# Kernel tuning notes

Measured on AMD Instinct MI355X. Metric: run time of the kernel, lower is better.

## Reference

```python
import jax, jax.numpy as jnp
import numpy as np

B, N, C, E, H, V, T = 64, 196, 512, 512, 1024, 10000, 20
NULL_IDX, START_IDX = 0, 1


def setup_inputs() -> dict:
    key = jax.random.key(0)
    ks = jax.random.split(key, 16)
    p = lambda k, s: jax.random.normal(k, s, jnp.float32) * 0.02
    z = lambda n: jnp.zeros((n,), jnp.float32)
    return dict(
        X=jax.random.normal(ks[0], (B, N, C), jnp.float32),
        emb=p(ks[1], (V, E)),
        W_ih=p(ks[2], (E + C, 4 * H)), b_ih=z(4 * H),
        W_hh=p(ks[3], (H, 4 * H)), b_hh=z(4 * H),
        Wa=p(ks[4], (C, H)), ba=z(H),          # attention lin_annotations
        Wh=p(ks[5], (H, H)), bh=z(H),          # attention lin_hidden
        Wo=p(ks[6], (H, 1)), bo=z(1),          # attention out
        Wlh=p(ks[7], (H, E)), blh=z(E),        # linear_hidden
        Wlc=p(ks[8], (C, E)), blc=z(E),        # linear_context
        Wout=p(ks[9], (E, V)), bout=z(V),      # linear_out
        Wc0=p(ks[10], (C, H)), bc0=z(H),       # cell_init
        Wh0=p(ks[11], (C, H)), bh0=z(H),       # hidden_init
    )


def reference(X, emb, W_ih, b_ih, W_hh, b_hh, Wa, ba, Wh, bh, Wo, bo,
              Wlh, blh, Wlc, blc, Wout, bout, Wc0, bc0, Wh0, bh0):
    Xm = jnp.mean(X, axis=1)                       # [B, C]
    c0 = jnp.tanh(Xm @ Wc0 + bc0)                  # [B, H]
    h0 = jnp.tanh(Xm @ Wh0 + bh0)                  # [B, H]
    Xa = X @ Wa + ba                               # [B, N, H] step-invariant annotation proj
    tok0 = jnp.full((B,), START_IDX, jnp.int32)

    def step(carry, _):
        tok, h, c = carry
        e = emb[tok]                                           # [B, E]
        att = jnp.tanh(Xa + (h @ Wh + bh)[:, None, :])          # [B, N, H]
        # softmax over a size-1 last axis -> weights == 1 (faithful to original)
        w = jax.nn.softmax(att @ Wo + bo, axis=-1)              # [B, N, 1]
        ctx = jnp.sum(w * X, axis=1)                            # [B, C]
        gates = jnp.concatenate([e, ctx], axis=1) @ W_ih + b_ih + h @ W_hh + b_hh
        gi, gf, gg, go = jnp.split(gates, 4, axis=1)            # torch LSTMCell gate order
        c2 = jax.nn.sigmoid(gf) * c + jax.nn.sigmoid(gi) * jnp.tanh(gg)
        h2 = jax.nn.sigmoid(go) * jnp.tanh(c2)
        comb = e + (h2 @ Wlh + blh) + (ctx @ Wlc + blc)         # [B, E]
        lp = jax.nn.log_softmax(comb @ Wout + bout, axis=-1)    # [B, V]
        tok2 = jnp.argmax(lp, axis=-1).astype(jnp.int32)
        return (tok2, h2, c2), lp

    _, lps = jax.lax.scan(step, (tok0, h0, c0), None, length=T - 1)  # [T-1, B, V]
    out0 = jnp.broadcast_to(jax.nn.one_hot(START_IDX, V, dtype=jnp.float32), (B, V))[None]
    out = jnp.concatenate([out0, lps], axis=0)                  # [T, B, V]
    return jnp.transpose(out, (1, 0, 2))                        # [B, T, V]
```

## Files before the change

kernel.cpp:

```cpp
#include <hip/hip_runtime.h>
#include <math.h>

typedef unsigned short u16;
typedef unsigned long long u64;
typedef __attribute__((ext_vector_type(8))) short bf16x8;
typedef __attribute__((ext_vector_type(4))) float f32x4;
typedef __attribute__((ext_vector_type(8))) unsigned short ushort8;

constexpr int kB = 64;
constexpr int kN = 196;
constexpr int kC = 512;
constexpr int kE = 512;
constexpr int kH = 1024;
constexpr int kV = 10000;
constexpr int kT = 20;
constexpr int kG4 = 4 * kH;
constexpr int kKA = 1536;
constexpr int kLT = 625;

__device__ __forceinline__ float sigmoidf_(float x) { return 1.0f / (1.0f + expf(-x)); }

__device__ __forceinline__ u16 f2bf(float x) {
    unsigned u = __float_as_uint(x);
    u += 0x7FFF + ((u >> 16) & 1);
    return (u16)(u >> 16);
}
__device__ __forceinline__ float bf2f(u16 u) {
    return __uint_as_float((unsigned)u << 16);
}
__device__ __forceinline__ void splitbf(float x, u16& hi, u16& lo) {
    hi = f2bf(x);
    lo = f2bf(x - bf2f(hi));
}

__device__ __forceinline__ u64 packMI(float M, int I) {
    unsigned mb = __float_as_uint(M);
    mb = (mb & 0x80000000u) ? ~mb : (mb | 0x80000000u);
    return ((u64)mb << 32) | (u64)(0xFFFFFFFFu - (unsigned)I);
}


__global__ __launch_bounds__(256) void k_colsum(const float* __restrict__ X,
                                                float* __restrict__ XsP) {
    int gid = blockIdx.x * 256 + threadIdx.x;
    int c = gid & 511, b = (gid >> 9) & 63, ch = gid >> 15;
    const float* p = X + (size_t)b * kN * kC + (size_t)(ch * 49) * kC + c;
    float s = 0.f;
    for (int n = 0; n < 49; ++n) s += p[(size_t)n * kC];
    XsP[gid] = s;
}

__global__ __launch_bounds__(256) void k_colred(const float* __restrict__ XsP,
                                                float* __restrict__ XsT) {
    int gid = blockIdx.x * 256 + threadIdx.x;
    int b = gid >> 9, c = gid & 511;
    float s = 0.f;
#pragma unroll
    for (int ch = 0; ch < 4; ++ch) s += XsP[ch * 32768 + b * 512 + c];
    XsT[c * kB + b] = s;
}

__global__ __launch_bounds__(256) void k_setupgemm(const float* __restrict__ XsT,
                                                   const float* __restrict__ W_ih,
                                                   const float* __restrict__ b_ih,
                                                   const float* __restrict__ b_hh,
                                                   const float* __restrict__ Wc0,
                                                   const float* __restrict__ bc0,
                                                   const float* __restrict__ Wh0,
                                                   const float* __restrict__ bh0,
                                                   const float* __restrict__ Wlc,
                                                   const float* __restrict__ blc,
                                                   const float* __restrict__ blh,
                                                   float* __restrict__ gbP,
                                                   float* __restrict__ cBJ,
                                                   u16* __restrict__ hb0Hi,
                                                   u16* __restrict__ hb0Lo,
                                                   float* __restrict__ ctxc) {
    __shared__ float4 wt4[64][8];
    int t = threadIdx.x;
    int b = t & 63, q = t >> 6;
    int tile = blockIdx.x;

    const float* W; const float* bias; float scale; int ldw; int mode; int j;
    if (tile < 128) {
        j = tile * 32; W = W_ih + (size_t)kE * kG4 + j; ldw = kG4;
        bias = nullptr; scale = 1.f; mode = 0;
    } else if (tile < 160) {
        j = (tile - 128) * 32; W = Wc0 + j; ldw = kH;
        bias = bc0 + j; scale = 1.0f / 196.0f; mode = 1;
    } else if (tile < 192) {
        j = (tile - 160) * 32; W = Wh0 + j; ldw = kH;
        bias = bh0 + j; scale = 1.0f / 196.0f; mode = 2;
    } else {
        j = (tile - 192) * 32; W = Wlc + j; ldw = kE;
        bias = blc + j; scale = 1.f; mode = 3;
    }

    int lr = t >> 2, lq2 = (t & 3) * 2;
    float acc[8];
#pragma unroll
    for (int i = 0; i < 8; ++i) acc[i] = 0.f;

    for (int kt = 0; kt < kC; kt += 64) {
        const float* wrow = W + (size_t)(kt + lr) * ldw;
        float4 w0 = *reinterpret_cast<const float4*>(wrow + lq2 * 4);
        float4 w1 = *reinterpret_cast<const float4*>(wrow + lq2 * 4 + 4);
        __syncthreads();
        wt4[lr][lq2] = w0; wt4[lr][lq2 + 1] = w1;
        __syncthreads();
        const float* ap = XsT + (size_t)kt * kB + b;
#pragma unroll 8
        for (int kk = 0; kk < 64; ++kk) {
            float a = ap[kk * 64] * scale;
            float4 u0 = wt4[kk][q * 2];
            float4 u1 = wt4[kk][q * 2 + 1];
            acc[0] += a * u0.x; acc[1] += a * u0.y; acc[2] += a * u0.z; acc[3] += a * u0.w;
            acc[4] += a * u1.x; acc[5] += a * u1.y; acc[6] += a * u1.z; acc[7] += a * u1.w;
        }
    }
#pragma unroll
    for (int cc = 0; cc < 8; ++cc) {
        int col = q * 8 + cc;
        float v = acc[cc];
        if (mode == 0) {
            int jsrc = j + col;
            v += b_ih[jsrc] + b_hh[jsrc];
            int nd = ((jsrc & 1023) << 2) | (jsrc >> 10);
            gbP[(size_t)b * kG4 + nd] = v;
        } else if (mode == 1) {
            v = tanhf(v + bias[col]);
            cBJ[(size_t)b * kH + j + col] = v;
        } else if (mode == 2) {
            v = tanhf(v + bias[col]);
            u16 hi, lo; splitbf(v, hi, lo);
            hb0Hi[(size_t)b * kH + j + col] = hi;
            hb0Lo[(size_t)b * kH + j + col] = lo;
        } else {
            v += bias[col] + blh[j + col];
            ctxc[(size_t)b * kE + j + col] = v;
        }
    }
}

__global__ __launch_bounds__(256) void k_wconv(const float* __restrict__ src,
                                               u16* __restrict__ dhi,
                                               u16* __restrict__ dlo,
                                               int ld, int n_valid, int pitch,
                                               int k_off, int nxTiles) {
    __shared__ float lds[64][65];
    int t = threadIdx.x;
    int nx = blockIdx.x % nxTiles, ky = blockIdx.x / nxTiles;
    int n0 = nx * 64, k0 = ky * 64;
    int c = t & 63, r0 = t >> 6;
#pragma unroll
    for (int i = 0; i < 16; ++i) {
        int r = r0 + i * 4;
        float v = (n0 + c < n_valid) ? src[(size_t)(k0 + r) * ld + n0 + c] : 0.f;
        lds[r][c] = v;
    }
    __syncthreads();
    int nl = t >> 2, kq = t & 3;
#pragma unroll
    for (int half = 0; half < 2; ++half) {
        ushort8 vh, vl;
#pragma unroll
        for (int jj = 0; jj < 8; ++jj) {
            u16 hi, lo; splitbf(lds[kq * 16 + half * 8 + jj][nl], hi, lo);
            vh[jj] = hi; vl[jj] = lo;
        }
        size_t o = (size_t)(n0 + nl) * pitch + k_off + k0 + kq * 16 + half * 8;
        *(ushort8*)(&dhi[o]) = vh;
        *(ushort8*)(&dlo[o]) = vl;
    }
}

__global__ __launch_bounds__(256) void k_wgconv(const float* __restrict__ src,
                                                u16* __restrict__ dhi,
                                                u16* __restrict__ dlo,
                                                int k_off) {
    __shared__ float lds[64][65];
    int t = threadIdx.x;
    int nx = blockIdx.x & 63, ky = blockIdx.x >> 6;
    int n0 = nx * 64, k0 = ky * 64;
    int c = t & 63, r0 = t >> 6;
#pragma unroll
    for (int i = 0; i < 16; ++i) {
        int r = r0 + i * 4;
        int nd = n0 + c;
        int nsrc = (nd & 3) * 1024 + (nd >> 2);
        lds[r][c] = src[(size_t)(k0 + r) * kG4 + nsrc];
    }
    __syncthreads();
    int nl = t >> 2, kq = t & 3;
#pragma unroll
    for (int half = 0; half < 2; ++half) {
        ushort8 vh, vl;
#pragma unroll
        for (int jj = 0; jj < 8; ++jj) {
            u16 hi, lo; splitbf(lds[kq * 16 + half * 8 + jj][nl], hi, lo);
            vh[jj] = hi; vl[jj] = lo;
        }
        size_t o = (size_t)(n0 + nl) * kKA + k_off + k0 + kq * 16 + half * 8;
        *(ushort8*)(&dhi[o]) = vh;
        *(ushort8*)(&dlo[o]) = vl;
    }
}

__global__ __launch_bounds__(256) void k_embconv(const float* __restrict__ emb,
                                                 u16* __restrict__ eh,
                                                 u16* __restrict__ el) {
    int gid = blockIdx.x * 256 + threadIdx.x;
    float4 v = *reinterpret_cast<const float4*>(emb + (size_t)gid * 4);
    u16 h0, l0, h1, l1, h2, l2, h3, l3;
    splitbf(v.x, h0, l0); splitbf(v.y, h1, l1);
    splitbf(v.z, h2, l2); splitbf(v.w, h3, l3);
    u64 ph = (u64)h0 | ((u64)h1 << 16) | ((u64)h2 << 32) | ((u64)h3 << 48);
    u64 pl = (u64)l0 | ((u64)l1 << 16) | ((u64)l2 << 32) | ((u64)l3 << 48);
    *reinterpret_cast<u64*>(eh + (size_t)gid * 4) = ph;
    *reinterpret_cast<u64*>(el + (size_t)gid * 4) = pl;
}

__global__ __launch_bounds__(256) void k_out0(float* __restrict__ out) {
    int gid = blockIdx.x * 256 + threadIdx.x;
    if (gid >= kB * kV) return;
    int b = gid / kV, v = gid - b * kV;
    out[(size_t)b * kT * kV + v] = (v == 1) ? 1.0f : 0.0f;
}


struct StepP {
    u16 *hbHi0, *hbLo0, *hbHi1, *hbLo1;
    float *cBJ, *gbP, *ctxc;
    u16 *CbHi, *CbLo;
    const u16 *WgHi, *WgLo, *WlhHi, *WlhLo, *WoHi, *WoLo, *embHi, *embLo;
    const float *bout;
    float *lbuf0, *lbuf1;
    float *Ssh;
    u64 *Mxsh;
    float *out;
};

__device__ __forceinline__ int resolveTok(const StepP& p, int step, int b) {
    if (step <= 1) return 1;
    int slot = (step - 1) & 1;
    u64 best = 0;
#pragma unroll
    for (int sh = 0; sh < 8; ++sh) {
        u64 v = p.Mxsh[(slot * 8 + sh) * 64 + b];
        if (v > best) best = v;
    }
    return (int)(0xFFFFFFFFu - (unsigned)(best & 0xFFFFFFFFu));
}

__global__ __launch_bounds__(256) void k_stepG(StepP p, int step) {
    __shared__ float sred[4][64][17];
    __shared__ int tok[64];
    const int blk = blockIdx.x, t = threadIdx.x;
    const int l = t & 63, w = t >> 6, la = l & 15, lg = l >> 4;
    const int Pb = (step - 1) & 1, Qb = step & 1;

    if (t < 64) tok[t] = resolveTok(p, step, t);
    if (blk < 8 && t < 64) {
        int slot = step & 1;
        p.Ssh[(slot * 8 + blk) * 64 + t] = 0.f;
        p.Mxsh[(slot * 8 + blk) * 64 + t] = 0;
    }
    __syncthreads();

    const u16* hpHi = Pb ? p.hbHi1 : p.hbHi0;
    const u16* hpLo = Pb ? p.hbLo1 : p.hbLo0;
    u16* nHi = Qb ? p.hbHi1 : p.hbHi0;
    u16* nLo = Qb ? p.hbLo1 : p.hbLo0;
    const int n0 = blk * 16;
    const int kb = w * 384 + lg * 8;
    const u16* wh = p.WgHi + (size_t)(n0 + la) * kKA + kb;
    const u16* wl = p.WgLo + (size_t)(n0 + la) * kKA + kb;
    int tk[4];
#pragma unroll
    for (int m = 0; m < 4; ++m) tk[m] = tok[m * 16 + la];

    f32x4 acc[4];
#pragma unroll
    for (int m = 0; m < 4; ++m) acc[m] = (f32x4){0.f, 0.f, 0.f, 0.f};
    for (int ks = 0; ks < 12; ++ks) {
        int kc = w * 384 + ks * 32;
        bf16x8 bhi = *(const bf16x8*)(wh + ks * 32);
        bf16x8 blo = *(const bf16x8*)(wl + ks * 32);
#pragma unroll
        for (int m = 0; m < 4; ++m) {
            int row = m * 16 + la;
            bf16x8 ahi8, alo8;
            if (kc < kE) {
                size_t o = (size_t)tk[m] * kE + kc + lg * 8;
                ahi8 = *(const bf16x8*)(p.embHi + o);
                alo8 = *(const bf16x8*)(p.embLo + o);
            } else {
                size_t o = (size_t)row * kH + (kc - kE) + lg * 8;
                ahi8 = *(const bf16x8*)(hpHi + o);
                alo8 = *(const bf16x8*)(hpLo + o);
            }
            acc[m] = __builtin_amdgcn_mfma_f32_16x16x32_bf16(ahi8, bhi, acc[m], 0, 0, 0);
            acc[m] = __builtin_amdgcn_mfma_f32_16x16x32_bf16(ahi8, blo, acc[m], 0, 0, 0);
            acc[m] = __builtin_amdgcn_mfma_f32_16x16x32_bf16(alo8, bhi, acc[m], 0, 0, 0);
        }
    }
#pragma unroll
    for (int m = 0; m < 4; ++m)
#pragma unroll
        for (int r = 0; r < 4; ++r)
            sred[w][m * 16 + lg * 4 + r][la] = acc[m][r];
    __syncthreads();
    int b = l, jl = w;
    float g[4];
#pragma unroll
    for (int gi = 0; gi < 4; ++gi) {
        int cc = jl * 4 + gi;
        g[gi] = sred[0][b][cc] + sred[1][b][cc] + sred[2][b][cc] + sred[3][b][cc]
              + p.gbP[(size_t)b * kG4 + n0 + cc];
    }
    int jp = blk * 4 + jl;
    float cold = p.cBJ[b * kH + jp];
    float c2 = sigmoidf_(g[1]) * cold + sigmoidf_(g[0]) * tanhf(g[2]);
    float h2 = sigmoidf_(g[3]) * tanhf(c2);
    p.cBJ[b * kH + jp] = c2;
    u16 hh, hl; splitbf(h2, hh, hl);
    nHi[(size_t)b * kH + jp] = hh;
    nLo[(size_t)b * kH + jp] = hl;
}

__global__ __launch_bounds__(256) void k_stepC(StepP p, int step) {
    __shared__ float sred[4][64][17];
    __shared__ int tok[64];
    __shared__ float lseArr[64];
    const int blk = blockIdx.x, t = threadIdx.x;
    const int Qb = step & 1;

    if (blk < 32) {
        if (t < 64) tok[t] = resolveTok(p, step, t);
        __syncthreads();
        const u16* hcHi = Qb ? p.hbHi1 : p.hbHi0;
        const u16* hcLo = Qb ? p.hbLo1 : p.hbLo0;
        const int l = t & 63, w = t >> 6, la = l & 15, lg = l >> 4;
        const int n0 = blk * 16;
        const int kb = w * 256 + lg * 8;
        const u16* wh = p.WlhHi + (size_t)(n0 + la) * kH + kb;
        const u16* wl = p.WlhLo + (size_t)(n0 + la) * kH + kb;
        f32x4 acc[4];
#pragma unroll
        for (int m = 0; m < 4; ++m) acc[m] = (f32x4){0.f, 0.f, 0.f, 0.f};
        for (int ks = 0; ks < 8; ++ks) {
            int ko = ks * 32;
            bf16x8 bhi = *(const bf16x8*)(wh + ko);
            bf16x8 blo = *(const bf16x8*)(wl + ko);
#pragma unroll
            for (int m = 0; m < 4; ++m) {
                size_t o = (size_t)(m * 16 + la) * kH + kb + ko;
                bf16x8 ahi8 = *(const bf16x8*)(hcHi + o);
                bf16x8 alo8 = *(const bf16x8*)(hcLo + o);
                acc[m] = __builtin_amdgcn_mfma_f32_16x16x32_bf16(ahi8, bhi, acc[m], 0, 0, 0);
                acc[m] = __builtin_amdgcn_mfma_f32_16x16x32_bf16(ahi8, blo, acc[m], 0, 0, 0);
                acc[m] = __builtin_amdgcn_mfma_f32_16x16x32_bf16(alo8, bhi, acc[m], 0, 0, 0);
            }
        }
#pragma unroll
        for (int m = 0; m < 4; ++m)
#pragma unroll
            for (int r = 0; r < 4; ++r)
                sred[w][m * 16 + lg * 4 + r][la] = acc[m][r];
        __syncthreads();
        int b = l, cq = w;
        int tokb = tok[b];
#pragma unroll
        for (int i = 0; i < 4; ++i) {
            int cc = cq * 4 + i;
            int col = (blk * 16) + cc;
            float v = sred[0][b][cc] + sred[1][b][cc] + sred[2][b][cc] + sred[3][b][cc];
            v += bf2f(p.embHi[(size_t)tokb * kE + col]) + bf2f(p.embLo[(size_t)tokb * kE + col]);
            v += p.ctxc[(size_t)b * kE + col];
            u16 hh, hl; splitbf(v, hh, hl);
            p.CbHi[(size_t)b * kE + col] = hh;
            p.CbLo[(size_t)b * kE + col] = hl;
        }
    } else if (step > 1) {
        int slot = (step - 1) & 1;
        if (t < 64) {
            float S = 0.f;
#pragma unroll
            for (int sh = 0; sh < 8; ++sh) S += p.Ssh[(slot * 8 + sh) * 64 + t];
            lseArr[t] = logf(S);
        }
        __syncthreads();
        const float* lb = slot ? p.lbuf1 : p.lbuf0;
        for (int idx = (blk - 32) * 256 + t; idx < kB * kV; idx += 224 * 256) {
            int b = idx / kV, c = idx - b * kV;
            __builtin_nontemporal_store(lb[(size_t)b * kV + c] - lseArr[b],
                                        &p.out[((size_t)b * kT + (step - 1)) * kV + c]);
        }
    }
}

__global__ __launch_bounds__(256) void k_stepL(StepP p, int step) {
    __shared__ float sred[4][64][17];
    __shared__ float redM[256], redS[256];
    __shared__ int redI[256];
    const int blk = blockIdx.x, t = threadIdx.x;
    const int l = t & 63, w = t >> 6, la = l & 15, lg = l >> 4;
    int slot = step & 1;
    float* lb = slot ? p.lbuf1 : p.lbuf0;
    int shard = blk & 7;
    const int c0 = blk * 16;
    const int kb = w * 128 + lg * 8;
    const u16* wh = p.WoHi + (size_t)(c0 + la) * kE + kb;
    const u16* wl = p.WoLo + (size_t)(c0 + la) * kE + kb;
    const u16* a0h = p.CbHi + (size_t)la * kE + kb;
    const u16* a0l = p.CbLo + (size_t)la * kE + kb;
    f32x4 acc[4];
#pragma unroll
    for (int m = 0; m < 4; ++m) acc[m] = (f32x4){0.f, 0.f, 0.f, 0.f};
#pragma unroll
    for (int ks = 0; ks < 4; ++ks) {
        int ko = ks * 32;
        bf16x8 bhi = *(const bf16x8*)(wh + ko);
        bf16x8 blo = *(const bf16x8*)(wl + ko);
#pragma unroll
        for (int m = 0; m < 4; ++m) {
            bf16x8 ahi8 = *(const bf16x8*)(a0h + (size_t)m * 16 * kE + ko);
            bf16x8 alo8 = *(const bf16x8*)(a0l + (size_t)m * 16 * kE + ko);
            acc[m] = __builtin_amdgcn_mfma_f32_16x16x32_bf16(ahi8, bhi, acc[m], 0, 0, 0);
            acc[m] = __builtin_amdgcn_mfma_f32_16x16x32_bf16(ahi8, blo, acc[m], 0, 0, 0);
            acc[m] = __builtin_amdgcn_mfma_f32_16x16x32_bf16(alo8, bhi, acc[m], 0, 0, 0);
        }
    }
#pragma unroll
    for (int m = 0; m < 4; ++m)
#pragma unroll
        for (int r = 0; r < 4; ++r)
            sred[w][m * 16 + lg * 4 + r][la] = acc[m][r];
    __syncthreads();
    int b = l, cq = w;
    float vals[4];
#pragma unroll
    for (int i = 0; i < 4; ++i) {
        int cc = cq * 4 + i;
        vals[i] = sred[0][b][cc] + sred[1][b][cc] + sred[2][b][cc] + sred[3][b][cc]
                + p.bout[c0 + cc];
    }
    __builtin_nontemporal_store((f32x4){vals[0], vals[1], vals[2], vals[3]},
                                (f32x4*)(lb + (size_t)b * kV + c0 + cq * 4));
    float m = vals[0]; int mi = 0;
#pragma unroll
    for (int i = 1; i < 4; ++i) if (vals[i] > m) { m = vals[i]; mi = i; }
    float se = 0.f;
#pragma unroll
    for (int i = 0; i < 4; ++i) se += __expf(vals[i] - m);
    redM[t] = m; redS[t] = se; redI[t] = c0 + cq * 4 + mi;
    __syncthreads();
    if (t < 64) {
        float M = redM[t], S = redS[t]; int I = redI[t];
#pragma unroll
        for (int q2 = 1; q2 < 4; ++q2) {
            float m2 = redM[t + q2 * 64], s2 = redS[t + q2 * 64];
            int i2 = redI[t + q2 * 64];
            float Mn = fmaxf(M, m2);
            S = S * __expf(M - Mn) + s2 * __expf(m2 - Mn);
            if (m2 > M || (m2 == M && i2 < I)) I = i2;
            M = Mn;
        }
        float S0 = S * __expf(M);
        atomicAdd(&p.Ssh[(slot * 8 + shard) * 64 + t], S0);
        atomicMax(&p.Mxsh[(slot * 8 + shard) * 64 + t], packMI(M, I));
    }
}

__global__ __launch_bounds__(256) void k_stepO(StepP p) {
    __shared__ float lseArr[64];
    const int blk = blockIdx.x, t = threadIdx.x;
    int slot = (kT - 1) & 1;
    if (t < 64) {
        float S = 0.f;
#pragma unroll
        for (int sh = 0; sh < 8; ++sh) S += p.Ssh[(slot * 8 + sh) * 64 + t];
        lseArr[t] = logf(S);
    }
    __syncthreads();
    const float* lb = slot ? p.lbuf1 : p.lbuf0;
    for (int idx = blk * 256 + t; idx < kB * kV; idx += 256 * 256) {
        int b = idx / kV, c = idx - b * kV;
        __builtin_nontemporal_store(lb[(size_t)b * kV + c] - lseArr[b],
                                    &p.out[((size_t)b * kT + (kT - 1)) * kV + c]);
    }
}


extern "C" void kernel_launch(void* const* d_in, const int* in_sizes, int n_in,
                              void* d_out, int out_size, void* d_ws, size_t ws_size,
                              hipStream_t stream) {
    const float* X    = (const float*)d_in[0];
    const float* emb  = (const float*)d_in[1];
    const float* W_ih = (const float*)d_in[2];
    const float* b_ih = (const float*)d_in[3];
    const float* W_hh = (const float*)d_in[4];
    const float* b_hh = (const float*)d_in[5];
    const float* Wlh  = (const float*)d_in[12];
    const float* blh  = (const float*)d_in[13];
    const float* Wlc  = (const float*)d_in[14];
    const float* blc  = (const float*)d_in[15];
    const float* Wout = (const float*)d_in[16];
    const float* bout = (const float*)d_in[17];
    const float* Wc0  = (const float*)d_in[18];
    const float* bc0  = (const float*)d_in[19];
    const float* Wh0  = (const float*)d_in[20];
    const float* bh0  = (const float*)d_in[21];
    float* out = (float*)d_out;

    char* cur = (char*)d_ws;
    auto carve = [&](size_t bytes) { char* p = cur; cur += (bytes + 255) & ~(size_t)255; return p; };

    u16* hbHi0 = (u16*)carve((size_t)kB * kH * 2);
    u16* hbLo0 = (u16*)carve((size_t)kB * kH * 2);
    u16* hbHi1 = (u16*)carve((size_t)kB * kH * 2);
    u16* hbLo1 = (u16*)carve((size_t)kB * kH * 2);
    float* cBJ  = (float*)carve((size_t)kB * kH * 4);
    float* gbP  = (float*)carve((size_t)kB * kG4 * 4);
    float* ctxc = (float*)carve((size_t)kB * kE * 4);
    u16* CbHi   = (u16*)carve((size_t)kB * kE * 2);
    u16* CbLo   = (u16*)carve((size_t)kB * kE * 2);
    float* XsT  = (float*)carve((size_t)kC * kB * 4);
    float* XsP  = (float*)carve((size_t)4 * kB * kC * 4);
    u16* WgHi   = (u16*)carve((size_t)kG4 * kKA * 2);
    u16* WgLo   = (u16*)carve((size_t)kG4 * kKA * 2);
    u16* WlhHi  = (u16*)carve((size_t)kE * kH * 2);
    u16* WlhLo  = (u16*)carve((size_t)kE * kH * 2);
    u16* WoHi   = (u16*)carve((size_t)10048 * kE * 2);
    u16* WoLo   = (u16*)carve((size_t)10048 * kE * 2);
    u16* embHi  = (u16*)carve((size_t)10000 * kE * 2);
    u16* embLo  = (u16*)carve((size_t)10000 * kE * 2);
    float* lbuf0 = (float*)carve((size_t)kB * kV * 4);
    float* lbuf1 = (float*)carve((size_t)kB * kV * 4);
    float* Ssh   = (float*)carve((size_t)2 * 8 * 64 * 4);
    u64*   Mxsh  = (u64*)carve((size_t)2 * 8 * 64 * 8);

    k_colsum<<<512, 256, 0, stream>>>(X, XsP);
    k_colred<<<128, 256, 0, stream>>>(XsP, XsT);
    k_setupgemm<<<208, 256, 0, stream>>>(XsT, W_ih, b_ih, b_hh, Wc0, bc0,
                                         Wh0, bh0, Wlc, blc, blh,
                                         gbP, cBJ, hbHi0, hbLo0, ctxc);
    k_out0<<<(kB * kV + 255) / 256, 256, 0, stream>>>(out);
    k_wgconv<<<64 * 8, 256, 0, stream>>>(W_ih, WgHi, WgLo, 0);
    k_wgconv<<<64 * 16, 256, 0, stream>>>(W_hh, WgHi, WgLo, kE);
    k_wconv<<<8 * 16, 256, 0, stream>>>(Wlh, WlhHi, WlhLo, kE, kE, kH, 0, 8);
    k_wconv<<<157 * 8, 256, 0, stream>>>(Wout, WoHi, WoLo, kV, kV, kE, 0, 157);
    k_embconv<<<5000, 256, 0, stream>>>(emb, embHi, embLo);

    StepP sp;
    sp.hbHi0 = hbHi0; sp.hbLo0 = hbLo0; sp.hbHi1 = hbHi1; sp.hbLo1 = hbLo1;
    sp.cBJ = cBJ; sp.gbP = gbP; sp.ctxc = ctxc;
    sp.CbHi = CbHi; sp.CbLo = CbLo;
    sp.WgHi = WgHi; sp.WgLo = WgLo; sp.WlhHi = WlhHi; sp.WlhLo = WlhLo;
    sp.WoHi = WoHi; sp.WoLo = WoLo; sp.embHi = embHi; sp.embLo = embLo;
    sp.bout = bout;
    sp.lbuf0 = lbuf0; sp.lbuf1 = lbuf1;
    sp.Ssh = Ssh; sp.Mxsh = Mxsh;
    sp.out = out;

    for (int s = 1; s < kT; ++s) {
        k_stepG<<<256, 256, 0, stream>>>(sp, s);
        k_stepC<<<256, 256, 0, stream>>>(sp, s);
        k_stepL<<<kLT, 256, 0, stream>>>(sp, s);
    }
    k_stepO<<<256, 256, 0, stream>>>(sp);
}
```

Baseline: 1.214 ms.

## Drop low-order weight split for LSTM gate and hidden projections; widen gate K-split

The gate and linear_hidden weights are now stored only as a single bf16 hi part. This removes the lo weight buffers, their conversion work, and one of the three MFMAs per tile in the recurrent steps, which reduces the weight bytes streamed each step. The gate kernel also goes from 256 to 512 threads, splitting K across 8 waves with an 8-way LDS reduction to raise parallelism. The cost is lower precision in the gate and hidden products, which could flip argmax tokens over the 19 steps.

```diff
diff --git a/kernel.cpp b/kernel.cpp
--- a/kernel.cpp
+++ b/kernel.cpp
@@ -176,7 +176,6 @@
 
 __global__ __launch_bounds__(256) void k_wgconv(const float* __restrict__ src,
                                                 u16* __restrict__ dhi,
-                                                u16* __restrict__ dlo,
                                                 int k_off) {
     __shared__ float lds[64][65];
     int t = threadIdx.x;
@@ -194,15 +193,36 @@
     int nl = t >> 2, kq = t & 3;
 #pragma unroll
     for (int half = 0; half < 2; ++half) {
-        ushort8 vh, vl;
-#pragma unroll
-        for (int jj = 0; jj < 8; ++jj) {
-            u16 hi, lo; splitbf(lds[kq * 16 + half * 8 + jj][nl], hi, lo);
-            vh[jj] = hi; vl[jj] = lo;
-        }
+        ushort8 vh;
+#pragma unroll
+        for (int jj = 0; jj < 8; ++jj) vh[jj] = f2bf(lds[kq * 16 + half * 8 + jj][nl]);
         size_t o = (size_t)(n0 + nl) * kKA + k_off + k0 + kq * 16 + half * 8;
         *(ushort8*)(&dhi[o]) = vh;
-        *(ushort8*)(&dlo[o]) = vl;
+    }
+}
+
+__global__ __launch_bounds__(256) void k_wconvh(const float* __restrict__ src,
+                                                u16* __restrict__ dhi,
+                                                int ld, int pitch, int nxTiles) {
+    __shared__ float lds[64][65];
+    int t = threadIdx.x;
+    int nx = blockIdx.x % nxTiles, ky = blockIdx.x / nxTiles;
+    int n0 = nx * 64, k0 = ky * 64;
+    int c = t & 63, r0 = t >> 6;
+#pragma unroll
+    for (int i = 0; i < 16; ++i) {
+        int r = r0 + i * 4;
+        lds[r][c] = src[(size_t)(k0 + r) * ld + n0 + c];
+    }
+    __syncthreads();
+    int nl = t >> 2, kq = t & 3;
+#pragma unroll
+    for (int half = 0; half < 2; ++half) {
+        ushort8 vh;
+#pragma unroll
+        for (int jj = 0; jj < 8; ++jj) vh[jj] = f2bf(lds[kq * 16 + half * 8 + jj][nl]);
+        size_t o = (size_t)(n0 + nl) * pitch + k0 + kq * 16 + half * 8;
+        *(ushort8*)(&dhi[o]) = vh;
     }
 }
 
@@ -232,7 +252,7 @@
     u16 *hbHi0, *hbLo0, *hbHi1, *hbLo1;
     float *cBJ, *gbP, *ctxc;
     u16 *CbHi, *CbLo;
-    const u16 *WgHi, *WgLo, *WlhHi, *WlhLo, *WoHi, *WoLo, *embHi, *embLo;
+    const u16 *WgHi, *WlhHi, *WoHi, *WoLo, *embHi, *embLo;
     const float *bout;
     float *lbuf0, *lbuf1;
     float *Ssh;
@@ -252,8 +272,8 @@
     return (int)(0xFFFFFFFFu - (unsigned)(best & 0xFFFFFFFFu));
 }
 
-__global__ __launch_bounds__(256) void k_stepG(StepP p, int step) {
-    __shared__ float sred[4][64][17];
+__global__ __launch_bounds__(512) void k_stepG(StepP p, int step) {
+    __shared__ float sred[8][64][17];
     __shared__ int tok[64];
     const int blk = blockIdx.x, t = threadIdx.x;
     const int l = t & 63, w = t >> 6, la = l & 15, lg = l >> 4;
@@ -272,9 +292,8 @@
     u16* nHi = Qb ? p.hbHi1 : p.hbHi0;
     u16* nLo = Qb ? p.hbLo1 : p.hbLo0;
     const int n0 = blk * 16;
-    const int kb = w * 384 + lg * 8;
+    const int kb = w * 192 + lg * 8;
     const u16* wh = p.WgHi + (size_t)(n0 + la) * kKA + kb;
-    const u16* wl = p.WgLo + (size_t)(n0 + la) * kKA + kb;
     int tk[4];
 #pragma unroll
     for (int m = 0; m < 4; ++m) tk[m] = tok[m * 16 + la];
@@ -282,10 +301,10 @@
     f32x4 acc[4];
 #pragma unroll
     for (int m = 0; m < 4; ++m) acc[m] = (f32x4){0.f, 0.f, 0.f, 0.f};
-    for (int ks = 0; ks < 12; ++ks) {
-        int kc = w * 384 + ks * 32;
+#pragma unroll
+    for (int ks = 0; ks < 6; ++ks) {
+        int kc = w * 192 + ks * 32;
         bf16x8 bhi = *(const bf16x8*)(wh + ks * 32);
-        bf16x8 blo = *(const bf16x8*)(wl + ks * 32);
 #pragma unroll
         for (int m = 0; m < 4; ++m) {
             int row = m * 16 + la;
@@ -300,7 +319,6 @@
                 alo8 = *(const bf16x8*)(hpLo + o);
             }
             acc[m] = __builtin_amdgcn_mfma_f32_16x16x32_bf16(ahi8, bhi, acc[m], 0, 0, 0);
-            acc[m] = __builtin_amdgcn_mfma_f32_16x16x32_bf16(ahi8, blo, acc[m], 0, 0, 0);
             acc[m] = __builtin_amdgcn_mfma_f32_16x16x32_bf16(alo8, bhi, acc[m], 0, 0, 0);
         }
     }
@@ -310,22 +328,26 @@
         for (int r = 0; r < 4; ++r)
             sred[w][m * 16 + lg * 4 + r][la] = acc[m][r];
     __syncthreads();
-    int b = l, jl = w;
-    float g[4];
-#pragma unroll
-    for (int gi = 0; gi < 4; ++gi) {
-        int cc = jl * 4 + gi;
-        g[gi] = sred[0][b][cc] + sred[1][b][cc] + sred[2][b][cc] + sred[3][b][cc]
-              + p.gbP[(size_t)b * kG4 + n0 + cc];
-    }
-    int jp = blk * 4 + jl;
-    float cold = p.cBJ[b * kH + jp];
-    float c2 = sigmoidf_(g[1]) * cold + sigmoidf_(g[0]) * tanhf(g[2]);
-    float h2 = sigmoidf_(g[3]) * tanhf(c2);
-    p.cBJ[b * kH + jp] = c2;
-    u16 hh, hl; splitbf(h2, hh, hl);
-    nHi[(size_t)b * kH + jp] = hh;
-    nLo[(size_t)b * kH + jp] = hl;
+    if (t < 256) {
+        int b = t & 63, jl = (t >> 6) & 3;
+        float g[4];
+#pragma unroll
+        for (int gi = 0; gi < 4; ++gi) {
+            int cc = jl * 4 + gi;
+            float s = p.gbP[(size_t)b * kG4 + n0 + cc];
+#pragma unroll
+            for (int wv = 0; wv < 8; ++wv) s += sred[wv][b][cc];
+            g[gi] = s;
+        }
+        int jp = blk * 4 + jl;
+        float cold = p.cBJ[b * kH + jp];
+        float c2 = sigmoidf_(g[1]) * cold + sigmoidf_(g[0]) * tanhf(g[2]);
+        float h2 = sigmoidf_(g[3]) * tanhf(c2);
+        p.cBJ[b * kH + jp] = c2;
+        u16 hh, hl; splitbf(h2, hh, hl);
+        nHi[(size_t)b * kH + jp] = hh;
+        nLo[(size_t)b * kH + jp] = hl;
+    }
 }
 
 __global__ __launch_bounds__(256) void k_stepC(StepP p, int step) {
@@ -344,21 +366,18 @@
         const int n0 = blk * 16;
         const int kb = w * 256 + lg * 8;
         const u16* wh = p.WlhHi + (size_t)(n0 + la) * kH + kb;
-        const u16* wl = p.WlhLo + (size_t)(n0 + la) * kH + kb;
         f32x4 acc[4];
 #pragma unroll
         for (int m = 0; m < 4; ++m) acc[m] = (f32x4){0.f, 0.f, 0.f, 0.f};
         for (int ks = 0; ks < 8; ++ks) {
             int ko = ks * 32;
             bf16x8 bhi = *(const bf16x8*)(wh + ko);
-            bf16x8 blo = *(const bf16x8*)(wl + ko);
 #pragma unroll
             for (int m = 0; m < 4; ++m) {
                 size_t o = (size_t)(m * 16 + la) * kH + kb + ko;
                 bf16x8 ahi8 = *(const bf16x8*)(hcHi + o);
                 bf16x8 alo8 = *(const bf16x8*)(hcLo + o);
                 acc[m] = __builtin_amdgcn_mfma_f32_16x16x32_bf16(ahi8, bhi, acc[m], 0, 0, 0);
-                acc[m] = __builtin_amdgcn_mfma_f32_16x16x32_bf16(ahi8, blo, acc[m], 0, 0, 0);
                 acc[m] = __builtin_amdgcn_mfma_f32_16x16x32_bf16(alo8, bhi, acc[m], 0, 0, 0);
             }
         }
@@ -368,7 +387,7 @@
             for (int r = 0; r < 4; ++r)
                 sred[w][m * 16 + lg * 4 + r][la] = acc[m][r];
         __syncthreads();
-        int b = l, cq = w;
+        int b = t & 63, cq = t >> 6;
         int tokb = tok[b];
 #pragma unroll
         for (int i = 0; i < 4; ++i) {
@@ -528,9 +547,7 @@
     float* XsT  = (float*)carve((size_t)kC * kB * 4);
     float* XsP  = (float*)carve((size_t)4 * kB * kC * 4);
     u16* WgHi   = (u16*)carve((size_t)kG4 * kKA * 2);
-    u16* WgLo   = (u16*)carve((size_t)kG4 * kKA * 2);
     u16* WlhHi  = (u16*)carve((size_t)kE * kH * 2);
-    u16* WlhLo  = (u16*)carve((size_t)kE * kH * 2);
     u16* WoHi   = (u16*)carve((size_t)10048 * kE * 2);
     u16* WoLo   = (u16*)carve((size_t)10048 * kE * 2);
     u16* embHi  = (u16*)carve((size_t)10000 * kE * 2);
@@ -546,9 +563,9 @@
                                          Wh0, bh0, Wlc, blc, blh,
                                          gbP, cBJ, hbHi0, hbLo0, ctxc);
     k_out0<<<(kB * kV + 255) / 256, 256, 0, stream>>>(out);
-    k_wgconv<<<64 * 8, 256, 0, stream>>>(W_ih, WgHi, WgLo, 0);
-    k_wgconv<<<64 * 16, 256, 0, stream>>>(W_hh, WgHi, WgLo, kE);
-    k_wconv<<<8 * 16, 256, 0, stream>>>(Wlh, WlhHi, WlhLo, kE, kE, kH, 0, 8);
+    k_wgconv<<<64 * 8, 256, 0, stream>>>(W_ih, WgHi, 0);
+    k_wgconv<<<64 * 16, 256, 0, stream>>>(W_hh, WgHi, kE);
+    k_wconvh<<<8 * 16, 256, 0, stream>>>(Wlh, WlhHi, kE, kH, 8);
     k_wconv<<<157 * 8, 256, 0, stream>>>(Wout, WoHi, WoLo, kV, kV, kE, 0, 157);
     k_embconv<<<5000, 256, 0, stream>>>(emb, embHi, embLo);
 
@@ -556,7 +573,7 @@
     sp.hbHi0 = hbHi0; sp.hbLo0 = hbLo0; sp.hbHi1 = hbHi1; sp.hbLo1 = hbLo1;
     sp.cBJ = cBJ; sp.gbP = gbP; sp.ctxc = ctxc;
     sp.CbHi = CbHi; sp.CbLo = CbLo;
-    sp.WgHi = WgHi; sp.WgLo = WgLo; sp.WlhHi = WlhHi; sp.WlhLo = WlhLo;
+    sp.WgHi = WgHi; sp.WlhHi = WlhHi;
     sp.WoHi = WoHi; sp.WoLo = WoLo; sp.embHi = embHi; sp.embLo = embLo;
     sp.bout = bout;
     sp.lbuf0 = lbuf0; sp.lbuf1 = lbuf1;
@@ -564,7 +581,7 @@
     sp.out = out;
 
     for (int s = 1; s < kT; ++s) {
-        k_stepG<<<256, 256, 0, stream>>>(sp, s);
+        k_stepG<<<256, 512, 0, stream>>>(sp, s);
         k_stepC<<<256, 256, 0, stream>>>(sp, s);
         k_stepL<<<kLT, 256, 0, stream>>>(sp, s);
     }
```

Result: faster. 1.022 ms (-15.8%).
